# Kernel optimization log

Measured on AMD Instinct MI355X. Metric: run time of the kernel, lower is better.

The kernel has to match this reference:

```python
import jax, jax.numpy as jnp
import numpy as np

V, D, H, KH, FF, E = 50257, 512, 8, 64, 2048, 4
B, S = 8, 1024


def _glorot(key, shape):
    # VarianceScaling(1.0, 'fan_avg') with normal-ish draw
    fan_in, fan_out = shape[-2], shape[-1]
    scale = np.sqrt(2.0 / (fan_in + fan_out)).astype(np.float32)
    return jax.random.normal(key, shape, dtype=jnp.float32) * scale


def _mha(x, Wq, Wk, Wv, Wo):
    # haiku MultiHeadAttention (self-attn, no mask, zero biases at init)
    b, s, _ = x.shape
    q = (x @ Wq).reshape(b, s, H, KH)
    k = (x @ Wk).reshape(b, s, H, KH)
    v = (x @ Wv).reshape(b, s, H, KH)
    logits = jnp.einsum('bthd,bThd->bhtT', q, k) / jnp.asarray(np.sqrt(KH), x.dtype)
    attn = jax.nn.softmax(logits, axis=-1)
    o = jnp.einsum('bhtT,bThd->bthd', attn, v).reshape(b, s, H * KH)
    return o @ Wo


def setup_inputs() -> dict:
    key = jax.random.key(0)
    ks = jax.random.split(key, 16)
    tokens = jax.random.randint(ks[0], (B, S), 0, V, dtype=jnp.int32)
    emb = jax.random.normal(ks[1], (V, D), dtype=jnp.float32) * 0.02
    Wq = _glorot(ks[2], (D, H * KH))
    Wk = _glorot(ks[3], (D, H * KH))
    Wv = _glorot(ks[4], (D, H * KH))
    Wo = _glorot(ks[5], (H * KH, D))
    W1 = _glorot(ks[6], (D, FF))
    W2 = _glorot(ks[7], (FF, D))
    Wg = _glorot(ks[8], (D, E))
    eWq = _glorot(ks[9], (E, D, H * KH))
    eWk = _glorot(ks[10], (E, D, H * KH))
    eWv = _glorot(ks[11], (E, D, H * KH))
    eWo = _glorot(ks[12], (E, H * KH, D))
    eW1 = _glorot(ks[13], (E, D, FF))
    eW2 = _glorot(ks[14], (E, FF, D))
    Wout = _glorot(ks[15], (D, 1))
    return dict(tokens=tokens, emb=emb, Wq=Wq, Wk=Wk, Wv=Wv, Wo=Wo, W1=W1, W2=W2,
                Wg=Wg, eWq=eWq, eWk=eWk, eWv=eWv, eWo=eWo, eW1=eW1, eW2=eW2, Wout=Wout)


def reference(tokens, emb, Wq, Wk, Wv, Wo, W1, W2, Wg, eWq, eWk, eWv, eWo, eW1, eW2, Wout):
    x = emb[tokens]                                     # [B,S,D] embedding gather
    h = (_mha(x, Wq, Wk, Wv, Wo) @ W1) @ W2             # shared transformer block
    gate = h @ Wg                                       # [B,S,E]
    idx = jnp.argmax(gate, axis=-1)                     # [B,S] per-token expert id
    out = jnp.zeros_like(h)
    for e in range(E):                                  # naive masked dense dispatch
        mask = (idx == e)[..., None]                    # [B,S,1]
        xe = jnp.where(mask, h, 0.0)
        ye = (_mha(xe, eWq[e], eWk[e], eWv[e], eWo[e]) @ eW1[e]) @ eW2[e]
        out = out + ye                                  # sum-aggregate expert outputs
    return out @ Wout                                   # [B,S,1]
```

## Files before the change

### kernel.cpp

```cpp
#include <hip/hip_runtime.h>
#include <stdint.h>
#include <stddef.h>

typedef __bf16 bf16_8 __attribute__((ext_vector_type(8)));
typedef float  f32x4  __attribute__((ext_vector_type(4)));

__device__ __forceinline__ unsigned short f2bf(float f) {
    unsigned u = __float_as_uint(f);
    unsigned r = (u + 0x7fffu + ((u >> 16) & 1u)) >> 16;
    return (unsigned short)r;
}
__device__ __forceinline__ float bf2f(unsigned short s) {
    return __uint_as_float(((unsigned)s) << 16);
}
__device__ __forceinline__ void split3(float v, unsigned short& h, unsigned short& l, unsigned short& l2) {
    h = f2bf(v);
    float r1 = v - bf2f(h);
    l = f2bf(r1);
    l2 = f2bf(r1 - bf2f(l));
}
__device__ __forceinline__ void split2(float v, unsigned short& h, unsigned short& l) {
    h = f2bf(v);
    l = f2bf(v - bf2f(h));
}

template<int P>
__global__ __launch_bounds__(256)
void wsplit_kernel(const float* __restrict__ s0, const float* __restrict__ s1,
                   const float* __restrict__ s2, const float* __restrict__ s3,
                   unsigned short* __restrict__ d0, unsigned short* __restrict__ d1,
                   unsigned short* __restrict__ d2, unsigned short* __restrict__ d3,
                   int K, int N, int nper, size_t sstride, size_t dstride)
{
    const int z = blockIdx.z;
    const int arr = z / nper, e = z - arr * nper;
    const float* src = (arr == 0 ? s0 : arr == 1 ? s1 : arr == 2 ? s2 : s3) + (size_t)e * sstride;
    unsigned short* dst = (arr == 0 ? d0 : arr == 1 ? d1 : arr == 2 ? d2 : d3) + (size_t)e * dstride;
    const size_t NK = (size_t)N * K;
    __shared__ float T[64][65];
    const int n0 = blockIdx.x * 64, k0 = blockIdx.y * 64;
    const int tid = threadIdx.x;
#pragma unroll
    for (int i = 0; i < 16; ++i) {
        int idx = tid + (i << 8);
        int kk = idx >> 6, nn = idx & 63;
        T[kk][nn] = src[(size_t)(k0 + kk) * N + n0 + nn];
    }
    __syncthreads();
#pragma unroll
    for (int i = 0; i < 4; ++i) {
        int idx = (tid + (i << 8)) << 2;
        int nn = idx >> 6, kk = idx & 63;
        ushort4 hv, lv, l2v;
        unsigned short* hp = (unsigned short*)&hv;
        unsigned short* lp = (unsigned short*)&lv;
        unsigned short* l2p = (unsigned short*)&l2v;
#pragma unroll
        for (int j = 0; j < 4; ++j) {
            float v = T[kk + j][nn];
            unsigned short h = f2bf(v);
            hp[j] = h;
            if (P == 3) {
                float r1 = v - bf2f(h);
                unsigned short l = f2bf(r1);
                lp[j] = l;
                l2p[j] = f2bf(r1 - bf2f(l));
            }
        }
        unsigned short* dp = dst + (size_t)(n0 + nn) * K + k0 + kk;
        *(ushort4*)dp = hv;
        if (P == 3) {
            *(ushort4*)(dp + NK) = lv;
            *(ushort4*)(dp + 2 * NK) = l2v;
        }
    }
}

template<int TERMS, int AMODE, int CMODE, int NW, int BPRE, int A16, int C16>
__global__ __launch_bounds__(256, 2)
void gemm_kernel(const void* __restrict__ Av,
                 const void* __restrict__ B0, const void* __restrict__ B1, const void* __restrict__ B2,
                 void* __restrict__ C0, void* __restrict__ C1, void* __restrict__ C2,
                 int M, int N, int K,
                 size_t astride, size_t bstride, size_t cstride,
                 const int* __restrict__ OFF, const int* __restrict__ flat)
{
    const int z = blockIdx.z;
    const int e = z / NW, w = z - e * NW;
    int base = 0, cnt = M;
    if (AMODE == 1 || AMODE == 2 || CMODE == 1 || CMODE == 2) {
        base = OFF[e * 8];
        cnt  = OFF[e * 8 + 8] - base;
        if ((int)blockIdx.x * 128 >= cnt) return;
    }
    const void* Bsel = (NW == 3 ? (w == 0 ? B0 : w == 1 ? B1 : B2) : B0);
    void*       Csel = (NW == 3 ? (w == 0 ? C0 : w == 1 ? C1 : C2) : C0);
    const float*          Af = (const float*)Av + (size_t)e * astride;
    const unsigned short* As = (const unsigned short*)Av;
    const float*          Bf = (const float*)Bsel + (size_t)e * bstride;
    const unsigned short* Bp = (const unsigned short*)Bsel + (size_t)e * bstride;
    float*          Cf = (float*)Csel + (size_t)e * cstride;
    unsigned short* Cs = (unsigned short*)Csel + (size_t)e * cstride;
    const size_t NKb = (size_t)N * K;

    constexpr int NPL = (TERMS == 6) ? 3 : 1;
    __shared__ unsigned short Asm[NPL][128 * 40];
    __shared__ unsigned short Bsm[NPL][128 * 40];

    const int tid   = threadIdx.x;
    const int lane  = tid & 63;
    const int wid   = tid >> 6;
    const int wm    = wid & 1, wn = wid >> 1;
    const int mlane = lane & 15, quad = lane >> 4;
    const int row0  = blockIdx.x * 128;
    const int col0  = blockIdx.y * 128;

    f32x4 acc[4][4];
#pragma unroll
    for (int i = 0; i < 4; ++i)
#pragma unroll
        for (int j = 0; j < 4; ++j)
#pragma unroll
            for (int r = 0; r < 4; ++r) acc[i][j][r] = 0.f;

    for (int k0 = 0; k0 < K; k0 += 32) {
        if (A16 == 0) {
#pragma unroll
            for (int i = 0; i < 4; ++i) {
                int idx = tid + (i << 8);
                int r = idx >> 3;
                int c = (idx & 7) << 2;
                int lr = row0 + r;
                if (AMODE != 0) lr = min(lr, cnt - 1);
                size_t arow = (AMODE == 2) ? (size_t)flat[base + lr]
                            : (AMODE == 1) ? (size_t)(base + lr) : (size_t)lr;
                const float4 a = *(const float4*)(Af + arow * K + k0 + c);
                float av[4] = {a.x, a.y, a.z, a.w};
                ushort4 hv, lv, l2v;
                unsigned short* hp  = (unsigned short*)&hv;
                unsigned short* lp  = (unsigned short*)&lv;
                unsigned short* l2p = (unsigned short*)&l2v;
#pragma unroll
                for (int j = 0; j < 4; ++j) {
                    unsigned short h = f2bf(av[j]);
                    hp[j] = h;
                    if (TERMS == 6) {
                        float r1 = av[j] - bf2f(h);
                        unsigned short l = f2bf(r1);
                        lp[j]  = l;
                        l2p[j] = f2bf(r1 - bf2f(l));
                    }
                }
                *(ushort4*)&Asm[0][r * 40 + c] = hv;
                if (TERMS == 6) {
                    *(ushort4*)&Asm[1][r * 40 + c] = lv;
                    *(ushort4*)&Asm[2][r * 40 + c] = l2v;
                }
            }
        } else {
#pragma unroll
            for (int j = 0; j < 2; ++j) {
                int c = tid * 2 + j;
                int r = c >> 2, q8 = (c & 3) << 3;
                int lr = row0 + r;
                if (AMODE != 0) lr = min(lr, cnt - 1);
                size_t arow = (AMODE == 2) ? (size_t)flat[base + lr]
                            : (AMODE == 1) ? (size_t)(base + lr) : (size_t)lr;
                *(uint4*)&Asm[0][r * 40 + q8] = *(const uint4*)(As + arow * K + k0 + q8);
            }
        }
        if (BPRE == 0) {
#pragma unroll
            for (int i = 0; i < 2; ++i) {
                int idx = tid + (i << 8);
                int kk = idx >> 4;
                int n8 = (idx & 15) << 3;
                const float* bp = Bf + (size_t)(k0 + kk) * N + col0 + n8;
                const float4 b0 = *(const float4*)bp;
                const float4 b1 = *(const float4*)(bp + 4);
                float bv[8] = {b0.x, b0.y, b0.z, b0.w, b1.x, b1.y, b1.z, b1.w};
#pragma unroll
                for (int j = 0; j < 8; ++j) {
                    unsigned short h = f2bf(bv[j]);
                    Bsm[0][(n8 + j) * 40 + kk] = h;
                    if (TERMS == 6) {
                        float r1 = bv[j] - bf2f(h);
                        unsigned short l = f2bf(r1);
                        Bsm[1][(n8 + j) * 40 + kk] = l;
                        Bsm[2][(n8 + j) * 40 + kk] = f2bf(r1 - bf2f(l));
                    }
                }
            }
        } else {
#pragma unroll
            for (int p = 0; p < NPL; ++p)
#pragma unroll
                for (int j = 0; j < 2; ++j) {
                    int c = tid * 2 + j;
                    int r = c >> 2, q8 = (c & 3) << 3;
                    *(uint4*)&Bsm[p][r * 40 + q8] =
                        *(const uint4*)(Bp + (size_t)p * NKb + (size_t)(col0 + r) * K + k0 + q8);
                }
        }
        __syncthreads();

        bf16_8 fa[3][4], fb[3][4];
#pragma unroll
        for (int t = 0; t < 4; ++t) {
            int ar = (wm * 64 + t * 16 + mlane) * 40 + quad * 8;
            int br = (wn * 64 + t * 16 + mlane) * 40 + quad * 8;
            fa[0][t] = *(const bf16_8*)&Asm[0][ar];
            fb[0][t] = *(const bf16_8*)&Bsm[0][br];
            if (TERMS == 6) {
                fa[1][t] = *(const bf16_8*)&Asm[1][ar];
                fa[2][t] = *(const bf16_8*)&Asm[2][ar];
                fb[1][t] = *(const bf16_8*)&Bsm[1][br];
                fb[2][t] = *(const bf16_8*)&Bsm[2][br];
            }
        }
        const int ta[6] = {0, 0, 1, 0, 1, 2};
        const int tb[6] = {0, 1, 0, 2, 1, 0};
#pragma unroll
        for (int s = 0; s < TERMS; ++s)
#pragma unroll
            for (int mt = 0; mt < 4; ++mt)
#pragma unroll
                for (int nt = 0; nt < 4; ++nt)
                    acc[mt][nt] = __builtin_amdgcn_mfma_f32_16x16x32_bf16(
                        fa[ta[s]][mt], fb[tb[s]][nt], acc[mt][nt], 0, 0, 0);
        __syncthreads();
    }

#pragma unroll
    for (int mt = 0; mt < 4; ++mt)
#pragma unroll
        for (int nt = 0; nt < 4; ++nt) {
            int c = col0 + wn * 64 + nt * 16 + mlane;
#pragma unroll
            for (int j = 0; j < 4; ++j) {
                int lr = row0 + wm * 64 + mt * 16 + quad * 4 + j;
                if ((CMODE == 1 || CMODE == 2) && lr >= cnt) continue;
                size_t crow = (CMODE == 2) ? (size_t)flat[base + lr]
                            : (CMODE == 1) ? (size_t)(base + lr) : (size_t)lr;
                if (C16) Cs[crow * N + c] = f2bf(acc[mt][nt][j]);
                else     Cf[crow * N + c] = acc[mt][nt][j];
            }
        }
}

__global__ __launch_bounds__(256)
void meanv_gemm_kernel(const float* __restrict__ in, const float* __restrict__ W,
                       float* __restrict__ out, int N, int K,
                       size_t instride, size_t wstride, size_t outstride)
{
    const int e  = blockIdx.z;
    const int nl = threadIdx.x & 63;
    const int kg = threadIdx.x >> 6;
    const int n  = blockIdx.x * 64 + nl;
    const int k0 = blockIdx.y * 512;

    const float* inp = in + (size_t)e * instride + k0;
    const float* wp  = W + (size_t)e * wstride + (size_t)(k0 + kg * 128) * N + n;

    __shared__ float mv[8][512];
    for (int i = threadIdx.x; i < 4096; i += 256) {
        int b = i >> 9, k = i & 511;
        mv[b][k] = inp[(size_t)b * K + k];
    }
    __syncthreads();

    float acc[8] = {0.f, 0.f, 0.f, 0.f, 0.f, 0.f, 0.f, 0.f};
#pragma unroll 8
    for (int k = 0; k < 128; ++k) {
        float wv = wp[(size_t)k * N];
        const float* mk = &mv[0][kg * 128 + k];
#pragma unroll
        for (int b = 0; b < 8; ++b) acc[b] += mk[b * 512] * wv;
    }

    __shared__ float red[4][8][64];
#pragma unroll
    for (int b = 0; b < 8; ++b) red[kg][b][nl] = acc[b];
    __syncthreads();
    if (kg == 0) {
        float* op = out + (size_t)e * outstride + n;
#pragma unroll
        for (int b = 0; b < 8; ++b) {
            float s = red[0][b][nl] + red[1][b][nl] + red[2][b][nl] + red[3][b][nl];
            if (gridDim.y == 1) op[(size_t)b * N] = s;
            else                atomicAdd(&op[(size_t)b * N], s);
        }
    }
}

__global__ __launch_bounds__(256, 2)
void attn_kernel(const float* __restrict__ Q, const float* __restrict__ Km,
                 const float* __restrict__ V, float* __restrict__ O)
{
    __shared__ __align__(16) unsigned short Ks[3][2][32][40];
    __shared__ __align__(16) unsigned short Vt[3][64][40];
    __shared__ __align__(16) unsigned short U[15360];

    const int tid = threadIdx.x;
    const int lane = tid & 63;
    const int w = tid >> 6;
    const int mlane = lane & 15, quad = lane >> 4;

    const int qt = blockIdx.x & 15;
    const int h  = (blockIdx.x >> 4) & 7;
    const int b  = blockIdx.x >> 7;
    const size_t rowbase = (size_t)b * 1024;
    const int colbase = h * 64;

#pragma unroll
    for (int i = 0; i < 4; ++i) {
        int idx = tid + (i << 8);
        int r = idx >> 4, c4 = (idx & 15) << 2;
        const float4 a = *(const float4*)(Q + (rowbase + qt * 64 + r) * 512 + colbase + c4);
        float av[4] = {a.x, a.y, a.z, a.w};
        ushort4 hv, lv, l2v;
        unsigned short* hp  = (unsigned short*)&hv;
        unsigned short* lp  = (unsigned short*)&lv;
        unsigned short* l2p = (unsigned short*)&l2v;
#pragma unroll
        for (int j = 0; j < 4; ++j) split3(av[j], hp[j], lp[j], l2p[j]);
        int ch = c4 >> 5, cm = c4 & 31;
        *(ushort4*)&U[(((0 * 2 + ch) * 64) + r) * 40 + cm] = hv;
        *(ushort4*)&U[(((1 * 2 + ch) * 64) + r) * 40 + cm] = lv;
        *(ushort4*)&U[(((2 * 2 + ch) * 64) + r) * 40 + cm] = l2v;
    }
    __syncthreads();

    bf16_8 fq[3][2];
#pragma unroll
    for (int p = 0; p < 3; ++p)
#pragma unroll
        for (int c = 0; c < 2; ++c)
            fq[p][c] = *(const bf16_8*)&U[(((p * 2 + c) * 64) + (w * 16 + mlane)) * 40 + quad * 8];
    __syncthreads();

    f32x4 oacc[4];
#pragma unroll
    for (int i = 0; i < 4; ++i)
#pragma unroll
        for (int j = 0; j < 4; ++j) oacc[i][j] = 0.f;
    float m_run = -1e30f, l_run = 0.f;

    const int ta[6] = {0, 0, 1, 0, 1, 2};
    const int tb[6] = {0, 1, 0, 2, 1, 0};

    for (int tt = 0; tt < 32; ++tt) {
        __syncthreads();
#pragma unroll
        for (int i = 0; i < 2; ++i) {
            int idx = tid + (i << 8);
            int r = idx >> 4, c4 = (idx & 15) << 2;
            const float4 a = *(const float4*)(Km + (rowbase + tt * 32 + r) * 512 + colbase + c4);
            float av[4] = {a.x, a.y, a.z, a.w};
            ushort4 hv, lv, l2v;
            unsigned short* hp  = (unsigned short*)&hv;
            unsigned short* lp  = (unsigned short*)&lv;
            unsigned short* l2p = (unsigned short*)&l2v;
#pragma unroll
            for (int j = 0; j < 4; ++j) split3(av[j], hp[j], lp[j], l2p[j]);
            int ch = c4 >> 5, cm = c4 & 31;
            *(ushort4*)&Ks[0][ch][r][cm] = hv;
            *(ushort4*)&Ks[1][ch][r][cm] = lv;
            *(ushort4*)&Ks[2][ch][r][cm] = l2v;
        }
#pragma unroll
        for (int i = 0; i < 2; ++i) {
            int idx = tid + (i << 8);
            int d = idx & 63, k4 = (idx >> 6) << 2;
            const float* vp = V + (rowbase + tt * 32 + k4) * 512 + colbase + d;
            float vv[4] = {vp[0], vp[512], vp[1024], vp[1536]};
            ushort4 hv, lv, l2v;
            unsigned short* hp  = (unsigned short*)&hv;
            unsigned short* lp  = (unsigned short*)&lv;
            unsigned short* l2p = (unsigned short*)&l2v;
#pragma unroll
            for (int j = 0; j < 4; ++j) split3(vv[j], hp[j], lp[j], l2p[j]);
            *(ushort4*)&Vt[0][d][k4] = hv;
            *(ushort4*)&Vt[1][d][k4] = lv;
            *(ushort4*)&Vt[2][d][k4] = l2v;
        }
        __syncthreads();

        f32x4 sacc[2];
#pragma unroll
        for (int mm = 0; mm < 2; ++mm)
#pragma unroll
            for (int j = 0; j < 4; ++j) sacc[mm][j] = 0.f;
        bf16_8 fk[3][2][2];
#pragma unroll
        for (int p = 0; p < 3; ++p)
#pragma unroll
            for (int c = 0; c < 2; ++c)
#pragma unroll
                for (int mm = 0; mm < 2; ++mm)
                    fk[p][c][mm] = *(const bf16_8*)&Ks[p][c][mm * 16 + mlane][quad * 8];
#pragma unroll
        for (int s = 0; s < 6; ++s)
#pragma unroll
            for (int c = 0; c < 2; ++c)
#pragma unroll
                for (int mm = 0; mm < 2; ++mm)
                    sacc[mm] = __builtin_amdgcn_mfma_f32_16x16x32_bf16(
                        fk[ta[s]][c][mm], fq[tb[s]][c], sacc[mm], 0, 0, 0);

        float sv[2][4];
#pragma unroll
        for (int mm = 0; mm < 2; ++mm)
#pragma unroll
            for (int j = 0; j < 4; ++j) sv[mm][j] = sacc[mm][j] * 0.125f;
        float tmax = sv[0][0];
#pragma unroll
        for (int mm = 0; mm < 2; ++mm)
#pragma unroll
            for (int j = 0; j < 4; ++j) tmax = fmaxf(tmax, sv[mm][j]);
        tmax = fmaxf(tmax, __shfl_xor(tmax, 16));
        tmax = fmaxf(tmax, __shfl_xor(tmax, 32));
        float mnew = fmaxf(m_run, tmax);
        float alpha = __expf(m_run - mnew);
        float lsum = 0.f;
#pragma unroll
        for (int mm = 0; mm < 2; ++mm)
#pragma unroll
            for (int j = 0; j < 4; ++j) {
                float p = __expf(sv[mm][j] - mnew);
                sv[mm][j] = p;
                lsum += p;
            }
        lsum += __shfl_xor(lsum, 16);
        lsum += __shfl_xor(lsum, 32);
        l_run = l_run * alpha + lsum;
        m_run = mnew;
#pragma unroll
        for (int mm = 0; mm < 4; ++mm)
#pragma unroll
            for (int j = 0; j < 4; ++j) oacc[mm][j] *= alpha;

#pragma unroll
        for (int mm = 0; mm < 2; ++mm) {
            ushort4 hv, lv, l2v;
            unsigned short* hp  = (unsigned short*)&hv;
            unsigned short* lp  = (unsigned short*)&lv;
            unsigned short* l2p = (unsigned short*)&l2v;
#pragma unroll
            for (int j = 0; j < 4; ++j) split3(sv[mm][j], hp[j], lp[j], l2p[j]);
            int col = mm * 16 + quad * 4;
            *(ushort4*)&U[((w * 3 + 0) * 16 + mlane) * 40 + col] = hv;
            *(ushort4*)&U[((w * 3 + 1) * 16 + mlane) * 40 + col] = lv;
            *(ushort4*)&U[((w * 3 + 2) * 16 + mlane) * 40 + col] = l2v;
        }

        bf16_8 fp[3], fv[3][4];
#pragma unroll
        for (int p = 0; p < 3; ++p) {
            fp[p] = *(const bf16_8*)&U[((w * 3 + p) * 16 + mlane) * 40 + quad * 8];
#pragma unroll
            for (int mm = 0; mm < 4; ++mm)
                fv[p][mm] = *(const bf16_8*)&Vt[p][mm * 16 + mlane][quad * 8];
        }
#pragma unroll
        for (int s = 0; s < 6; ++s)
#pragma unroll
            for (int mm = 0; mm < 4; ++mm)
                oacc[mm] = __builtin_amdgcn_mfma_f32_16x16x32_bf16(
                    fv[ta[s]][mm], fp[tb[s]], oacc[mm], 0, 0, 0);
    }

    const float inv = 1.f / l_run;
    const size_t orow = (rowbase + qt * 64 + w * 16 + mlane) * 512 + colbase;
#pragma unroll
    for (int mm = 0; mm < 4; ++mm)
#pragma unroll
        for (int j = 0; j < 4; ++j)
            O[orow + mm * 16 + quad * 4 + j] = oacc[mm][j] * inv;
}

__global__ __launch_bounds__(256, 3)
void attn_compact_kernel(const float* __restrict__ Qc, const float* __restrict__ Kc,
                         const float* __restrict__ Vc, const float* __restrict__ meanV,
                         unsigned short* __restrict__ AOc, const int* __restrict__ OFF)
{
    const int qt = blockIdx.x & 15;
    const int h  = (blockIdx.x >> 4) & 7;
    const int e  = (blockIdx.x >> 7) & 3;
    const int b  = blockIdx.x >> 9;
    const int base = OFF[e * 8 + b];
    const int c    = OFF[e * 8 + b + 1] - base;
    if (qt * 64 >= c) return;
    const int nq = min(64, c - qt * 64);

    __shared__ __align__(16) unsigned short Ks[2][2][32][40];
    __shared__ __align__(16) unsigned short Vt[2][64][40];
    __shared__ __align__(16) unsigned short U[10240];

    const int tid = threadIdx.x;
    const int lane = tid & 63;
    const int w = tid >> 6;
    const int mlane = lane & 15, quad = lane >> 4;
    const int colbase = h * 64;
    const int cmax = c - 1;

#pragma unroll
    for (int i = 0; i < 4; ++i) {
        int idx = tid + (i << 8);
        int r = idx >> 4, c4 = (idx & 15) << 2;
        const size_t g = (size_t)(base + min(qt * 64 + r, cmax)) * 512 + colbase + c4;
        const float4 a = *(const float4*)(Qc + g);
        float av[4] = {a.x, a.y, a.z, a.w};
        ushort4 hv, lv;
        unsigned short* hp = (unsigned short*)&hv;
        unsigned short* lp = (unsigned short*)&lv;
#pragma unroll
        for (int j = 0; j < 4; ++j) split2(av[j], hp[j], lp[j]);
        int ch = c4 >> 5, cm = c4 & 31;
        *(ushort4*)&U[(((0 * 2 + ch) * 64) + r) * 40 + cm] = hv;
        *(ushort4*)&U[(((1 * 2 + ch) * 64) + r) * 40 + cm] = lv;
    }
    __syncthreads();

    bf16_8 fq[2][2];
#pragma unroll
    for (int p = 0; p < 2; ++p)
#pragma unroll
        for (int cc = 0; cc < 2; ++cc)
            fq[p][cc] = *(const bf16_8*)&U[(((p * 2 + cc) * 64) + (w * 16 + mlane)) * 40 + quad * 8];
    __syncthreads();

    f32x4 oacc[4];
#pragma unroll
    for (int i = 0; i < 4; ++i)
#pragma unroll
        for (int j = 0; j < 4; ++j) oacc[i][j] = 0.f;
    float m_run = -1e30f, l_run = 0.f;

    const int ta3[3] = {0, 0, 1};
    const int tb3[3] = {0, 1, 0};

    for (int kt = 0; kt * 32 < c; ++kt) {
        __syncthreads();
#pragma unroll
        for (int i = 0; i < 2; ++i) {
            int idx = tid + (i << 8);
            int r = idx >> 4, c4 = (idx & 15) << 2;
            const size_t g = (size_t)(base + min(kt * 32 + r, cmax)) * 512 + colbase + c4;
            const float4 a = *(const float4*)(Kc + g);
            float av[4] = {a.x, a.y, a.z, a.w};
            ushort4 hv, lv;
            unsigned short* hp = (unsigned short*)&hv;
            unsigned short* lp = (unsigned short*)&lv;
#pragma unroll
            for (int j = 0; j < 4; ++j) split2(av[j], hp[j], lp[j]);
            int ch = c4 >> 5, cm = c4 & 31;
            *(ushort4*)&Ks[0][ch][r][cm] = hv;
            *(ushort4*)&Ks[1][ch][r][cm] = lv;
        }
#pragma unroll
        for (int i = 0; i < 2; ++i) {
            int idx = tid + (i << 8);
            int d = idx & 63, k4 = (idx >> 6) << 2;
            float vv[4];
#pragma unroll
            for (int j = 0; j < 4; ++j)
                vv[j] = Vc[(size_t)(base + min(kt * 32 + k4 + j, cmax)) * 512 + colbase + d];
            ushort4 hv, lv;
            unsigned short* hp = (unsigned short*)&hv;
            unsigned short* lp = (unsigned short*)&lv;
#pragma unroll
            for (int j = 0; j < 4; ++j) split2(vv[j], hp[j], lp[j]);
            *(ushort4*)&Vt[0][d][k4] = hv;
            *(ushort4*)&Vt[1][d][k4] = lv;
        }
        __syncthreads();

        f32x4 sacc[2];
#pragma unroll
        for (int mm = 0; mm < 2; ++mm)
#pragma unroll
            for (int j = 0; j < 4; ++j) sacc[mm][j] = 0.f;
        bf16_8 fk[2][2][2];
#pragma unroll
        for (int p = 0; p < 2; ++p)
#pragma unroll
            for (int cc = 0; cc < 2; ++cc)
#pragma unroll
                for (int mm = 0; mm < 2; ++mm)
                    fk[p][cc][mm] = *(const bf16_8*)&Ks[p][cc][mm * 16 + mlane][quad * 8];
#pragma unroll
        for (int s = 0; s < 3; ++s)
#pragma unroll
            for (int cc = 0; cc < 2; ++cc)
#pragma unroll
                for (int mm = 0; mm < 2; ++mm)
                    sacc[mm] = __builtin_amdgcn_mfma_f32_16x16x32_bf16(
                        fk[ta3[s]][cc][mm], fq[tb3[s]][cc], sacc[mm], 0, 0, 0);

        float sv[2][4];
#pragma unroll
        for (int mm = 0; mm < 2; ++mm)
#pragma unroll
            for (int j = 0; j < 4; ++j) {
                int kg = kt * 32 + mm * 16 + quad * 4 + j;
                sv[mm][j] = (kg < c) ? sacc[mm][j] * 0.125f : -1e30f;
            }
        float tmax = sv[0][0];
#pragma unroll
        for (int mm = 0; mm < 2; ++mm)
#pragma unroll
            for (int j = 0; j < 4; ++j) tmax = fmaxf(tmax, sv[mm][j]);
        tmax = fmaxf(tmax, __shfl_xor(tmax, 16));
        tmax = fmaxf(tmax, __shfl_xor(tmax, 32));
        float mnew = fmaxf(m_run, tmax);
        float alpha = __expf(m_run - mnew);
        float lsum = 0.f;
#pragma unroll
        for (int mm = 0; mm < 2; ++mm)
#pragma unroll
            for (int j = 0; j < 4; ++j) {
                float p = __expf(sv[mm][j] - mnew);
                sv[mm][j] = p;
                lsum += p;
            }
        lsum += __shfl_xor(lsum, 16);
        lsum += __shfl_xor(lsum, 32);
        l_run = l_run * alpha + lsum;
        m_run = mnew;
#pragma unroll
        for (int mm = 0; mm < 4; ++mm)
#pragma unroll
            for (int j = 0; j < 4; ++j) oacc[mm][j] *= alpha;

#pragma unroll
        for (int mm = 0; mm < 2; ++mm) {
            ushort4 hv, lv;
            unsigned short* hp = (unsigned short*)&hv;
            unsigned short* lp = (unsigned short*)&lv;
#pragma unroll
            for (int j = 0; j < 4; ++j) split2(sv[mm][j], hp[j], lp[j]);
            int col = mm * 16 + quad * 4;
            *(ushort4*)&U[((w * 2 + 0) * 16 + mlane) * 40 + col] = hv;
            *(ushort4*)&U[((w * 2 + 1) * 16 + mlane) * 40 + col] = lv;
        }

        bf16_8 fp[2], fv[2][4];
#pragma unroll
        for (int p = 0; p < 2; ++p) {
            fp[p] = *(const bf16_8*)&U[((w * 2 + p) * 16 + mlane) * 40 + quad * 8];
#pragma unroll
            for (int mm = 0; mm < 4; ++mm)
                fv[p][mm] = *(const bf16_8*)&Vt[p][mm * 16 + mlane][quad * 8];
        }
#pragma unroll
        for (int s = 0; s < 3; ++s)
#pragma unroll
            for (int mm = 0; mm < 4; ++mm)
                oacc[mm] = __builtin_amdgcn_mfma_f32_16x16x32_bf16(
                    fv[ta3[s]][mm], fp[tb3[s]], oacc[mm], 0, 0, 0);
    }

    float mfin = (c < 1024) ? fmaxf(m_run, 0.f) : m_run;
    float alphaf = __expf(m_run - mfin);
    l_run = l_run * alphaf + (float)(1024 - c) * __expf(-mfin);
#pragma unroll
    for (int mm = 0; mm < 4; ++mm)
#pragma unroll
        for (int j = 0; j < 4; ++j) oacc[mm][j] *= alphaf;

    const int qi = w * 16 + mlane;
    if (qi < nq) {
        const float inv = 1.f / l_run;
        const size_t orow = (size_t)(base + qt * 64 + qi) * 512 + colbase;
        const float* mv = meanV + e * 65536 + b * 512 + colbase;
#pragma unroll
        for (int mm = 0; mm < 4; ++mm) {
            int d0 = mm * 16 + quad * 4;
            ushort4 o;
            o.x = f2bf(oacc[mm][0] * inv - mv[d0 + 0]);
            o.y = f2bf(oacc[mm][1] * inv - mv[d0 + 1]);
            o.z = f2bf(oacc[mm][2] * inv - mv[d0 + 2]);
            o.w = f2bf(oacc[mm][3] * inv - mv[d0 + 3]);
            *(ushort4*)&AOc[orow + d0] = o;
        }
    }
}

__global__ void sumv_kernel(const float* __restrict__ Vc, const int* __restrict__ OFF,
                            float* __restrict__ M32)
{
    const int h = blockIdx.x & 7, e = (blockIdx.x >> 3) & 3, b = blockIdx.x >> 5;
    const int base = OFF[e * 8 + b], c = OFF[e * 8 + b + 1] - base;
    const int tid = threadIdx.x;
    const int d = tid & 63, g = tid >> 6;
    float s = 0.f;
    for (int r = g; r < c; r += 4) s += Vc[(size_t)(base + r) * 512 + h * 64 + d];
    __shared__ float red[256];
    red[tid] = s;
    __syncthreads();
    if (g == 0)
        M32[e * 65536 + b * 512 + h * 64 + d] =
            (red[d] + red[64 + d] + red[128 + d] + red[192 + d]) * (1.f / 1024.f);
}

__global__ void gather_kernel(const int* __restrict__ tokens,
                              const float* __restrict__ emb,
                              float* __restrict__ X)
{
    const int t = blockIdx.x;
    const int tok = tokens[t];
    const float4* src = (const float4*)(emb + (size_t)tok * 512);
    float4* dst = (float4*)(X + (size_t)t * 512);
    dst[threadIdx.x] = src[threadIdx.x];
}

__global__ __launch_bounds__(256)
void gate_kernel(const float* __restrict__ H, const float* __restrict__ Wg,
                 int* __restrict__ idx)
{
    const int t = blockIdx.x * 4 + (threadIdx.x >> 6);
    const int lane = threadIdx.x & 63;
    float a0 = 0, a1 = 0, a2 = 0, a3 = 0;
#pragma unroll
    for (int i = 0; i < 8; ++i) {
        int d = i * 64 + lane;
        float hv = H[(size_t)t * 512 + d];
        a0 += hv * Wg[d * 4 + 0];
        a1 += hv * Wg[d * 4 + 1];
        a2 += hv * Wg[d * 4 + 2];
        a3 += hv * Wg[d * 4 + 3];
    }
#pragma unroll
    for (int off = 32; off > 0; off >>= 1) {
        a0 += __shfl_down(a0, off);
        a1 += __shfl_down(a1, off);
        a2 += __shfl_down(a2, off);
        a3 += __shfl_down(a3, off);
    }
    if (lane == 0) {
        int best = 0; float bv = a0;
        if (a1 > bv) { bv = a1; best = 1; }
        if (a2 > bv) { bv = a2; best = 2; }
        if (a3 > bv) { bv = a3; best = 3; }
        idx[t] = best;
    }
}

__global__ void count_kernel(const int* __restrict__ idx, int* __restrict__ cnt)
{
    const int t = blockIdx.x * 256 + threadIdx.x;
    atomicAdd(&cnt[idx[t] * 8 + (t >> 10)], 1);
}
__global__ void offsets_kernel(const int* __restrict__ cnt, int* __restrict__ OFF,
                               int* __restrict__ cursor)
{
    if (threadIdx.x == 0) {
        int a = 0;
        for (int i = 0; i < 32; ++i) { OFF[i] = a; cursor[i] = a; a += cnt[i]; }
        OFF[32] = a;
    }
}
__global__ void fill_kernel(const int* __restrict__ idx, int* __restrict__ cursor,
                            int* __restrict__ flat)
{
    const int t = blockIdx.x * 256 + threadIdx.x;
    const int p = atomicAdd(&cursor[idx[t] * 8 + (t >> 10)], 1);
    flat[p] = t;
}

__global__ void sb_kernel(const float* __restrict__ G2, const float* __restrict__ Wout,
                          float* __restrict__ SB)
{
    const int tid = threadIdx.x;
    const int pair = tid >> 3, t8 = tid & 7;
    const int e = pair >> 3, b = pair & 7;
    float s = 0.f;
    for (int d = t8; d < 512; d += 8) s += G2[e * 65536 + b * 512 + d] * Wout[d];
    __shared__ float red[256];
    __shared__ float red2[32];
    red[tid] = s;
    __syncthreads();
    if (tid < 32) {
        float t = 0.f;
#pragma unroll
        for (int k = 0; k < 8; ++k) t += red[tid * 8 + k];
        red2[tid] = t;
    }
    __syncthreads();
    if (tid < 8)
        SB[tid] = red2[tid] + red2[8 + tid] + red2[16 + tid] + red2[24 + tid];
}

__global__ __launch_bounds__(256)
void wout_kernel(const float* __restrict__ OUT, const float* __restrict__ Wout,
                 const float* __restrict__ SB, float* __restrict__ out)
{
    const int t = blockIdx.x * 4 + (threadIdx.x >> 6);
    const int lane = threadIdx.x & 63;
    float s = 0.f;
#pragma unroll
    for (int i = 0; i < 8; ++i) {
        int d = i * 64 + lane;
        s += OUT[(size_t)t * 512 + d] * Wout[d];
    }
#pragma unroll
    for (int off = 32; off > 0; off >>= 1) s += __shfl_down(s, off);
    if (lane == 0) out[t] = s + SB[t >> 10];
}

extern "C" void kernel_launch(void* const* d_in, const int* in_sizes, int n_in,
                              void* d_out, int out_size, void* d_ws, size_t ws_size,
                              hipStream_t stream)
{
    const int*   tokens = (const int*)d_in[0];
    const float* emb  = (const float*)d_in[1];
    const float* Wq   = (const float*)d_in[2];
    const float* Wk   = (const float*)d_in[3];
    const float* Wv   = (const float*)d_in[4];
    const float* Wo   = (const float*)d_in[5];
    const float* W1   = (const float*)d_in[6];
    const float* W2   = (const float*)d_in[7];
    const float* Wg   = (const float*)d_in[8];
    const float* eWq  = (const float*)d_in[9];
    const float* eWk  = (const float*)d_in[10];
    const float* eWv  = (const float*)d_in[11];
    const float* eWo  = (const float*)d_in[12];
    const float* eW1  = (const float*)d_in[13];
    const float* eW2  = (const float*)d_in[14];
    const float* Wout = (const float*)d_in[15];
    float* outp = (float*)d_out;

    float* WS = (float*)d_ws;
    const size_t SZ = (size_t)8192 * 512;
    float* P0 = WS, *P1 = WS + SZ, *P2 = WS + 2 * SZ, *P3 = WS + 3 * SZ, *P4 = WS + 4 * SZ;

    unsigned short* SP   = (unsigned short*)(WS + 5 * SZ);
    unsigned short* sW1p = SP;
    unsigned short* sW2p = SP + 3145728;
    unsigned short* xWq  = SP + 6291456;
    unsigned short* xWk  = xWq + 1048576;
    unsigned short* xWv  = xWk + 1048576;
    unsigned short* xWo  = xWv + 1048576;
    unsigned short* xW1  = xWo + 1048576;
    unsigned short* xW2  = xW1 + 4194304;

    float* MBase = WS + 5 * SZ + 9437184;
    int* IDX    = (int*)MBase;
    int* cnt    = (int*)(MBase + 8192);
    int* OFFp   = (int*)(MBase + 8224);
    int* cursor = (int*)(MBase + 8264);
    int* flat   = (int*)(MBase + 8304);
    float* M32  = MBase + 16640;
    float* G0   = M32 + 262144;
    float* G2   = G0 + 262144;
    float* SB   = G2 + 262144;

    float* X = P4, *Qb = P0, *Kb = P1, *Vb = P2, *AO = P3, *T0 = P4, *T1 = P0, *Hb = P4;
    float* Qc = P0, *Kc = P1, *Vc = P2;
    unsigned short* AOc = (unsigned short*)P3;
    unsigned short* T0c = (unsigned short*)(P3 + 2097152);
    unsigned short* T1c = (unsigned short*)P0;
    float* G1 = P2;
    float* OA = P3;

    const int M = 8192, D = 512, FF = 2048;
    const size_t sDD = (size_t)D * D, sDF = (size_t)D * FF;
    const float* NUL = nullptr;
    float* NULm = nullptr;

    wsplit_kernel<3><<<dim3(32, 8, 1),  256, 0, stream>>>(W1, NUL, NUL, NUL, sW1p, 0, 0, 0, D, FF, 1, 0, 0);
    wsplit_kernel<3><<<dim3(8, 32, 1),  256, 0, stream>>>(W2, NUL, NUL, NUL, sW2p, 0, 0, 0, FF, D, 1, 0, 0);
    wsplit_kernel<1><<<dim3(8, 8, 16),  256, 0, stream>>>(eWq, eWk, eWv, eWo, xWq, xWk, xWv, xWo, D, D, 4, sDD, 262144);
    wsplit_kernel<1><<<dim3(32, 8, 4),  256, 0, stream>>>(eW1, NUL, NUL, NUL, xW1, 0, 0, 0, D, FF, 4, sDF, 1048576);
    wsplit_kernel<1><<<dim3(8, 32, 4),  256, 0, stream>>>(eW2, NUL, NUL, NUL, xW2, 0, 0, 0, FF, D, 4, sDF, 1048576);

    gather_kernel<<<8192, 128, 0, stream>>>(tokens, emb, X);
    gemm_kernel<6, 0, 0, 3, 0, 0, 0><<<dim3(64, 4, 3), 256, 0, stream>>>(
        X, Wq, Wk, Wv, Qb, Kb, Vb, M, D, D, 0, 0, 0, nullptr, nullptr);
    attn_kernel<<<1024, 256, 0, stream>>>(Qb, Kb, Vb, AO);
    gemm_kernel<6, 0, 0, 1, 0, 0, 0><<<dim3(64, 4, 1), 256, 0, stream>>>(
        AO, Wo, NUL, NUL, T0, NULm, NULm, M, D, D, 0, 0, 0, nullptr, nullptr);
    gemm_kernel<6, 0, 0, 1, 1, 0, 0><<<dim3(64, 16, 1), 256, 0, stream>>>(
        T0, sW1p, NUL, NUL, T1, NULm, NULm, M, FF, D, 0, 0, 0, nullptr, nullptr);
    gemm_kernel<6, 0, 0, 1, 1, 0, 0><<<dim3(64, 4, 1), 256, 0, stream>>>(
        T1, sW2p, NUL, NUL, Hb, NULm, NULm, M, D, FF, 0, 0, 0, nullptr, nullptr);
    gate_kernel<<<2048, 256, 0, stream>>>(Hb, Wg, IDX);

    hipMemsetAsync(cnt, 0, 32 * sizeof(int), stream);
    hipMemsetAsync(M32, 0, 4 * 128 * 512 * sizeof(float), stream);
    hipMemsetAsync(G2, 0, 262144 * sizeof(float), stream);
    count_kernel<<<32, 256, 0, stream>>>(IDX, cnt);
    offsets_kernel<<<1, 64, 0, stream>>>(cnt, OFFp, cursor);
    fill_kernel<<<32, 256, 0, stream>>>(IDX, cursor, flat);

    gemm_kernel<1, 2, 1, 3, 1, 0, 0><<<dim3(64, 4, 12), 256, 0, stream>>>(
        Hb, xWq, xWk, xWv, Qc, Kc, Vc, M, D, D, 0, 262144, 0, OFFp, flat);
    sumv_kernel<<<256, 256, 0, stream>>>(Vc, OFFp, M32);
    attn_compact_kernel<<<4096, 256, 0, stream>>>(Qc, Kc, Vc, M32, AOc, OFFp);

    gemm_kernel<1, 1, 1, 1, 1, 1, 1><<<dim3(64, 4, 4), 256, 0, stream>>>(
        AOc, xWo, NUL, NUL, T0c, NULm, NULm, M, D, D, 0, 262144, 0, OFFp, flat);
    gemm_kernel<1, 1, 1, 1, 1, 1, 1><<<dim3(64, 16, 4), 256, 0, stream>>>(
        T0c, xW1, NUL, NUL, T1c, NULm, NULm, M, FF, D, 0, 1048576, 0, OFFp, flat);

    meanv_gemm_kernel<<<dim3(8, 1, 4),  256, 0, stream>>>(M32, eWo, G0, 512,  512,  65536,  sDD, 65536);
    meanv_gemm_kernel<<<dim3(32, 1, 4), 256, 0, stream>>>(G0,  eW1, G1, 2048, 512,  65536,  sDF, 262144);
    meanv_gemm_kernel<<<dim3(8, 4, 4),  256, 0, stream>>>(G1,  eW2, G2, 512,  2048, 262144, sDF, 65536);

    gemm_kernel<1, 1, 2, 1, 1, 1, 0><<<dim3(64, 4, 4), 256, 0, stream>>>(
        T1c, xW2, NUL, NUL, OA, NULm, NULm, M, D, FF, 0, 1048576, 0, OFFp, flat);

    sb_kernel<<<1, 256, 0, stream>>>(G2, Wout, SB);
    wout_kernel<<<2048, 256, 0, stream>>>(OA, Wout, SB, outp);
}
```

Baseline: 1.510 ms.

## Pre-split embedding gather and shared attention weights into bf16 planes for GEMMs

The gather kernel now writes the embedding rows as three bf16 split planes (hi/lo/lo2) instead of fp32, and the QKV GEMM reads these pre-split A planes through a new NPL/astride path. The shared Wq/Wk/Wv/Wo weights are also pre-split with a dedicated wsplit launch, so the QKV and Wo GEMMs skip the per-tile fp32-to-bf16 conversion of operands. The expert weight split that reuses the same buffers is moved after the Wo GEMM. This trades extra memory traffic for the planar X (three bf16 planes versus one fp32) against less conversion arithmetic inside the GEMM inner loops.

Result: faster. 1.384 ms (-8.3%).

```diff
diff --git a/kernel.cpp b/kernel.cpp
--- a/kernel.cpp
+++ b/kernel.cpp
@@ -159,15 +159,18 @@
             }
         } else {
 #pragma unroll
-            for (int j = 0; j < 2; ++j) {
-                int c = tid * 2 + j;
-                int r = c >> 2, q8 = (c & 3) << 3;
-                int lr = row0 + r;
-                if (AMODE != 0) lr = min(lr, cnt - 1);
-                size_t arow = (AMODE == 2) ? (size_t)flat[base + lr]
-                            : (AMODE == 1) ? (size_t)(base + lr) : (size_t)lr;
-                *(uint4*)&Asm[0][r * 40 + q8] = *(const uint4*)(As + arow * K + k0 + q8);
-            }
+            for (int p = 0; p < NPL; ++p)
+#pragma unroll
+                for (int j = 0; j < 2; ++j) {
+                    int c = tid * 2 + j;
+                    int r = c >> 2, q8 = (c & 3) << 3;
+                    int lr = row0 + r;
+                    if (AMODE != 0) lr = min(lr, cnt - 1);
+                    size_t arow = (AMODE == 2) ? (size_t)flat[base + lr]
+                                : (AMODE == 1) ? (size_t)(base + lr) : (size_t)lr;
+                    *(uint4*)&Asm[p][r * 40 + q8] =
+                        *(const uint4*)(As + (size_t)p * astride + arow * K + k0 + q8);
+                }
         }
         if (BPRE == 0) {
 #pragma unroll
@@ -706,13 +709,23 @@
 
 __global__ void gather_kernel(const int* __restrict__ tokens,
                               const float* __restrict__ emb,
-                              float* __restrict__ X)
+                              unsigned short* __restrict__ Xp)
 {
     const int t = blockIdx.x;
     const int tok = tokens[t];
-    const float4* src = (const float4*)(emb + (size_t)tok * 512);
-    float4* dst = (float4*)(X + (size_t)t * 512);
-    dst[threadIdx.x] = src[threadIdx.x];
+    const int d4 = threadIdx.x * 4;
+    const float4 a = *(const float4*)(emb + (size_t)tok * 512 + d4);
+    float av[4] = {a.x, a.y, a.z, a.w};
+    ushort4 hv, lv, l2v;
+    unsigned short* hp  = (unsigned short*)&hv;
+    unsigned short* lp  = (unsigned short*)&lv;
+    unsigned short* l2p = (unsigned short*)&l2v;
+#pragma unroll
+    for (int j = 0; j < 4; ++j) split3(av[j], hp[j], lp[j], l2p[j]);
+    const size_t o = (size_t)t * 512 + d4;
+    *(ushort4*)&Xp[o]           = hv;
+    *(ushort4*)&Xp[o + 4194304] = lv;
+    *(ushort4*)&Xp[o + 8388608] = l2v;
 }
 
 __global__ __launch_bounds__(256)
@@ -856,7 +869,8 @@
     float* G2   = G0 + 262144;
     float* SB   = G2 + 262144;
 
-    float* X = P4, *Qb = P0, *Kb = P1, *Vb = P2, *AO = P3, *T0 = P4, *T1 = P0, *Hb = P4;
+    float* Qb = P0, *Kb = P1, *Vb = P2, *AO = P3, *T0 = P4, *T1 = P0, *Hb = P4;
+    unsigned short* Xp = (unsigned short*)P3;
     float* Qc = P0, *Kc = P1, *Vc = P2;
     unsigned short* AOc = (unsigned short*)P3;
     unsigned short* T0c = (unsigned short*)(P3 + 2097152);
@@ -871,16 +885,17 @@
 
     wsplit_kernel<3><<<dim3(32, 8, 1),  256, 0, stream>>>(W1, NUL, NUL, NUL, sW1p, 0, 0, 0, D, FF, 1, 0, 0);
     wsplit_kernel<3><<<dim3(8, 32, 1),  256, 0, stream>>>(W2, NUL, NUL, NUL, sW2p, 0, 0, 0, FF, D, 1, 0, 0);
-    wsplit_kernel<1><<<dim3(8, 8, 16),  256, 0, stream>>>(eWq, eWk, eWv, eWo, xWq, xWk, xWv, xWo, D, D, 4, sDD, 262144);
+    wsplit_kernel<3><<<dim3(8, 8, 4),   256, 0, stream>>>(Wq, Wk, Wv, Wo, xWq, xWk, xWv, xWo, D, D, 1, 0, 0);
     wsplit_kernel<1><<<dim3(32, 8, 4),  256, 0, stream>>>(eW1, NUL, NUL, NUL, xW1, 0, 0, 0, D, FF, 4, sDF, 1048576);
     wsplit_kernel<1><<<dim3(8, 32, 4),  256, 0, stream>>>(eW2, NUL, NUL, NUL, xW2, 0, 0, 0, FF, D, 4, sDF, 1048576);
 
-    gather_kernel<<<8192, 128, 0, stream>>>(tokens, emb, X);
-    gemm_kernel<6, 0, 0, 3, 0, 0, 0><<<dim3(64, 4, 3), 256, 0, stream>>>(
-        X, Wq, Wk, Wv, Qb, Kb, Vb, M, D, D, 0, 0, 0, nullptr, nullptr);
+    gather_kernel<<<8192, 128, 0, stream>>>(tokens, emb, Xp);
+    gemm_kernel<6, 0, 0, 3, 1, 1, 0><<<dim3(64, 4, 3), 256, 0, stream>>>(
+        Xp, xWq, xWk, xWv, Qb, Kb, Vb, M, D, D, (size_t)M * D, 0, 0, nullptr, nullptr);
     attn_kernel<<<1024, 256, 0, stream>>>(Qb, Kb, Vb, AO);
-    gemm_kernel<6, 0, 0, 1, 0, 0, 0><<<dim3(64, 4, 1), 256, 0, stream>>>(
-        AO, Wo, NUL, NUL, T0, NULm, NULm, M, D, D, 0, 0, 0, nullptr, nullptr);
+    gemm_kernel<6, 0, 0, 1, 1, 0, 0><<<dim3(64, 4, 1), 256, 0, stream>>>(
+        AO, xWo, NUL, NUL, T0, NULm, NULm, M, D, D, 0, 0, 0, nullptr, nullptr);
+    wsplit_kernel<1><<<dim3(8, 8, 16),  256, 0, stream>>>(eWq, eWk, eWv, eWo, xWq, xWk, xWv, xWo, D, D, 4, sDD, 262144);
     gemm_kernel<6, 0, 0, 1, 1, 0, 0><<<dim3(64, 16, 1), 256, 0, stream>>>(
         T0, sW1p, NUL, NUL, T1, NULm, NULm, M, FF, D, 0, 0, 0, nullptr, nullptr);
     gemm_kernel<6, 0, 0, 1, 1, 0, 0><<<dim3(64, 4, 1), 256, 0, stream>>>(
```
